# Optimization experiments

Hardware: AMD Instinct MI355X
Metric: run time of the kernel (lower is better)

Reference implementation:

```python
import jax, jax.numpy as jnp
import numpy as np

N, G, HID, LAT, E_RAND = 20000, 3000, 256, 32, 320000
EPS = 1e-8
NEG_SLOPE = 0.2  # PyG GATv2Conv default leaky_relu slope


def _segment_softmax(logits, seg, n):
    # numerically stable softmax over edges grouped by destination node
    m = jax.ops.segment_max(logits, seg, num_segments=n)
    ex = jnp.exp(logits - m[seg])
    s = jax.ops.segment_sum(ex, seg, num_segments=n)
    return ex / (s[seg] + 1e-16)


def _gatv2(x, src, dst, Wl, Wr, att, b, n):
    # GATv2 (heads=1): score = att . leaky_relu(Wl x_j + Wr x_i)
    xl = x @ Wl  # [N, C] source transform (also the message)
    xr = x @ Wr  # [N, C] destination transform
    e = jax.nn.leaky_relu(xl[src] + xr[dst], NEG_SLOPE)  # [E, C]
    logit = e @ att  # [E]
    alpha = _segment_softmax(logit, dst, n)
    out = jax.ops.segment_sum(alpha[:, None] * xl[src], dst, num_segments=n)
    return out + b


def _log_zinb(x, mu, theta, pi):
    theta = theta[None, :]
    softplus_pi = jax.nn.softplus(-pi)
    log_theta_eps = jnp.log(theta + EPS)
    log_theta_mu_eps = jnp.log(theta + mu + EPS)
    pi_theta_log = -pi + theta * (log_theta_eps - log_theta_mu_eps)
    case_zero = jax.nn.softplus(pi_theta_log) - softplus_pi
    case_nz = (-softplus_pi + pi_theta_log
               + x * (jnp.log(mu + EPS) - log_theta_mu_eps)
               + jax.lax.lgamma(x + theta) - jax.lax.lgamma(theta)
               - jax.lax.lgamma(x + 1.0))
    return jnp.where(x < EPS, case_zero, 0.0) + jnp.where(x > EPS, case_nz, 0.0)


def setup_inputs():
    key = jax.random.key(0)
    ks = jax.random.split(key, 14)
    x = jax.random.randint(ks[0], (N, G), 0, 20).astype(jnp.float32)
    er = jax.random.randint(ks[1], (2, E_RAND), 0, N, dtype=jnp.int32)
    loops = jnp.tile(jnp.arange(N, dtype=jnp.int32)[None, :], (2, 1))
    edge_index = jnp.concatenate([er, loops], axis=1)  # [2, 340000] incl self-loops
    noise = jax.random.normal(ks[2], (N, LAT), dtype=jnp.float32)

    def init(k, shape, fan_in):
        return jax.random.normal(k, shape, dtype=jnp.float32) / np.float32(np.sqrt(fan_in))

    Wl1 = init(ks[3], (G, HID), G); Wr1 = init(ks[4], (G, HID), G)
    att1 = init(ks[5], (HID,), HID); b1 = jnp.zeros((HID,), jnp.float32)
    Wl2 = init(ks[6], (HID, 2 * LAT), HID); Wr2 = init(ks[7], (HID, 2 * LAT), HID)
    att2 = init(ks[8], (2 * LAT,), 2 * LAT); b2 = jnp.zeros((2 * LAT,), jnp.float32)
    Wd1 = init(ks[9], (LAT, HID), LAT); bd1 = jnp.zeros((HID,), jnp.float32)
    Wd2 = init(ks[10], (HID, G), HID); bd2 = jnp.zeros((G,), jnp.float32)
    Wdo = init(ks[11], (HID, G), HID); bdo = jnp.zeros((G,), jnp.float32)
    theta = jax.random.uniform(ks[12], (G,), minval=0.5, maxval=2.0, dtype=jnp.float32)
    return dict(x=x, edge_index=edge_index, noise=noise,
                Wl1=Wl1, Wr1=Wr1, att1=att1, b1=b1,
                Wl2=Wl2, Wr2=Wr2, att2=att2, b2=b2,
                Wd1=Wd1, bd1=bd1, Wd2=Wd2, bd2=bd2, Wdo=Wdo, bdo=bdo,
                theta=theta)


def reference(x, edge_index, noise, Wl1, Wr1, att1, b1, Wl2, Wr2, att2, b2,
              Wd1, bd1, Wd2, bd2, Wdo, bdo, theta):
    n = x.shape[0]
    src, dst = edge_index[0], edge_index[1]
    # --- GATv2 encoder ---
    h = _gatv2(x, src, dst, Wl1, Wr1, att1, b1, n)
    h2 = _gatv2(jax.nn.relu(h), src, dst, Wl2, Wr2, att2, b2, n)  # [N, 2*LAT]
    mu_z, logvar = h2[:, :LAT], h2[:, LAT:]
    # --- reparameterize: std = sqrt(exp(logvar)) ---
    z = mu_z + noise * jnp.exp(0.5 * logvar)
    # --- ZINB decoder ---
    hd = z @ Wd1 + bd1
    mean = jax.nn.softplus(hd @ Wd2 + bd2)
    pi = hd @ Wdo + bdo
    # --- loss: -E[log ZINB] + KL(q(z|x) || N(0,I)) ---
    recon = -jnp.mean(jnp.sum(_log_zinb(x, mean, theta, pi), axis=1))
    kl = jnp.mean(0.5 * jnp.sum(mu_z ** 2 + jnp.exp(logvar) - logvar - 1.0, axis=1))
    return recon + kl
```

## Files before the change

kernel.cpp:

```cpp
#include <hip/hip_runtime.h>
#include <math.h>

#define NN   20000
#define GG   3000
#define HIDD 256
#define LATT 32
#define KP1  3008
#define FEPS 1e-8f

typedef __attribute__((ext_vector_type(8))) __bf16 bf16x8;
typedef __attribute__((ext_vector_type(4))) float f32x4;

__device__ __forceinline__ float fsp(float v) {
    float t = __expf(-fabsf(v));
    return fmaxf(v, 0.f) + __logf(1.f + t);
}
__device__ __forceinline__ float sp_approx(float t) {
    float a = fabsf(t);
    float den = fmaf(a, fmaf(a, fmaf(a, 0.8382f, -1.4958f), 1.87f), 1.f);
    return fmaxf(t, 0.f) + 0.6931472f * __builtin_amdgcn_rcpf(den);
}
__device__ __forceinline__ float lrelu(float v) {
    return v > 0.f ? v : 0.2f * v;
}
__device__ __forceinline__ ushort f2bf(float f) {
    uint b = __float_as_uint(f);
    return (ushort)((b + 0x7FFFu + ((b >> 16) & 1u)) >> 16);
}
__device__ __forceinline__ float bf2f(ushort u) {
    return __uint_as_float((uint)u << 16);
}
__device__ __forceinline__ uint pk2(float a, float b) {
    return (uint)f2bf(a) | ((uint)f2bf(b) << 16);
}
__device__ __forceinline__ void gload16(const void* g, void* l) {
    __builtin_amdgcn_global_load_lds((const __attribute__((address_space(1))) void*)g,
                                     (__attribute__((address_space(3))) void*)l, 16, 0, 0);
}

__global__ __launch_bounds__(256)
void x2bf(const float* __restrict__ x, ushort* __restrict__ xb) {
    const size_t nch = (size_t)NN * (GG / 8);
    size_t i = (size_t)blockIdx.x * 256 + threadIdx.x;
    if (i >= nch) return;
    size_t row = i / (GG / 8);
    int c8 = (int)(i % (GG / 8)) * 8;
    const float* p = x + row * GG + c8;
    float4 a = ((const float4*)p)[0];
    float4 b = ((const float4*)p)[1];
    uint4 w;
    w.x = pk2(a.x, a.y); w.y = pk2(a.z, a.w);
    w.z = pk2(b.x, b.y); w.w = pk2(b.z, b.w);
    *(uint4*)(xb + row * GG + c8) = w;
}

__global__ void zinb_table(const float* __restrict__ theta, float* __restrict__ tabL,
                           float* __restrict__ logte, int G_) {
    int idx = blockIdx.x * blockDim.x + threadIdx.x;
    if (idx >= G_ * 20) return;
    int g = idx / 20, c = idx % 20;
    float th = theta[g];
    tabL[idx] = lgammaf((float)c + th) - lgammaf(th) - lgammaf((float)c + 1.f);
    if (c == 0) logte[g] = logf(th + FEPS);
}

__global__ void edge_hist(const int* __restrict__ ei, int* __restrict__ cnt, int E) {
    int e = blockIdx.x * blockDim.x + threadIdx.x;
    if (e < E) atomicAdd(&cnt[ei[E + e]], 1);
}

__global__ __launch_bounds__(1024)
void scan_deg(int* __restrict__ cnt_cur, int* __restrict__ rowptr, int Nn) {
    __shared__ int ts[1024];
    int t = threadIdx.x;
    int chunk = (Nn + 1023) / 1024;
    int beg = t * chunk, end = min(beg + chunk, Nn);
    int s = 0;
    for (int i = beg; i < end; i++) s += cnt_cur[i];
    ts[t] = s;
    __syncthreads();
    for (int off = 1; off < 1024; off <<= 1) {
        int v = (t >= off) ? ts[t - off] : 0;
        __syncthreads();
        ts[t] += v;
        __syncthreads();
    }
    int run = (t == 0) ? 0 : ts[t - 1];
    for (int i = beg; i < end; i++) {
        int c = cnt_cur[i];
        rowptr[i] = run;
        cnt_cur[i] = run;
        run += c;
    }
    if (t == 1023) rowptr[Nn] = ts[1023];
}

__global__ void edge_scatter(const int* __restrict__ ei, int* __restrict__ cur,
                             int* __restrict__ eidx, int E) {
    int e = blockIdx.x * blockDim.x + threadIdx.x;
    if (e < E) {
        int p = atomicAdd(&cur[ei[E + e]], 1);
        eidx[p] = e;
    }
}

__global__ __launch_bounds__(256)
void transp_bf16(const float* __restrict__ in, ushort* __restrict__ out,
                 int K, int N, int Kpad) {
    __shared__ ushort t[32][33];
    int k0 = blockIdx.x * 32, n0 = blockIdx.y * 32;
    int tx = threadIdx.x & 31, ty = threadIdx.x >> 5;
    #pragma unroll
    for (int u = 0; u < 32; u += 8) {
        int k = k0 + ty + u, n = n0 + tx;
        t[ty + u][tx] = (k < K && n < N) ? f2bf(in[(size_t)k * N + n]) : (ushort)0;
    }
    __syncthreads();
    #pragma unroll
    for (int u = 0; u < 32; u += 8) {
        int n = n0 + ty + u, k = k0 + tx;
        if (n < N && k < Kpad) out[(size_t)n * Kpad + k] = t[tx][ty + u];
    }
}

__global__ __launch_bounds__(256)
void wcomb(const float* __restrict__ Wd1, const float* __restrict__ bd1,
           const float* __restrict__ Wd2, const float* __restrict__ bd2,
           const float* __restrict__ Wdo, const float* __restrict__ bdo,
           ushort* __restrict__ W2t, ushort* __restrict__ Wot,
           float* __restrict__ b2c, float* __restrict__ boc, int G_) {
    __shared__ float w1s[32 * 256];
    int tid = threadIdx.x;
    for (int i = tid; i < 32 * 256; i += 256) w1s[i] = Wd1[i];
    __syncthreads();
    int gl = tid & 63, rg = tid >> 6;
    int g = blockIdx.x * 64 + gl;
    int gc = min(g, G_ - 1);
    float a2[8], ao[8];
    #pragma unroll
    for (int i = 0; i < 8; i++) { a2[i] = 0.f; ao[i] = 0.f; }
    float ab2 = 0.f, abo = 0.f;
    for (int j = 0; j < 256; j++) {
        float w2 = Wd2[(size_t)j * G_ + gc];
        float wo = Wdo[(size_t)j * G_ + gc];
        if (rg == 0) {
            float b1 = bd1[j];
            ab2 = fmaf(b1, w2, ab2);
            abo = fmaf(b1, wo, abo);
        }
        #pragma unroll
        for (int i = 0; i < 8; i++) {
            float w1 = w1s[(rg * 8 + i) * 256 + j];
            a2[i] = fmaf(w1, w2, a2[i]);
            ao[i] = fmaf(w1, wo, ao[i]);
        }
    }
    if (g < G_) {
        #pragma unroll
        for (int i = 0; i < 8; i++) {
            W2t[(size_t)g * 32 + rg * 8 + i] = f2bf(a2[i]);
            Wot[(size_t)g * 32 + rg * 8 + i] = f2bf(ao[i]);
        }
        if (rg == 0) { b2c[g] = ab2 + bd2[g]; boc[g] = abo + bdo[g]; }
    }
}

__global__ __launch_bounds__(256, 4)
void dec_zinb(const ushort* __restrict__ zb, const ushort* __restrict__ W2t,
              const ushort* __restrict__ Wot, const ushort* __restrict__ xb,
              const float* __restrict__ tabL, const float* __restrict__ theta,
              const float* __restrict__ logte, const float* __restrict__ b2c,
              const float* __restrict__ boc, double* __restrict__ partsR,
              int M, int G_) {
    __shared__ float tabs[64 * 20];
    __shared__ float thetas[64], thltes[64], bd2s[64], bdos[64];
    __shared__ double redd[4];
    const int tid = threadIdx.x;
    const int nwg = gridDim.x * gridDim.y;
    const int orig = blockIdx.y * gridDim.x + blockIdx.x;
    const int q = nwg >> 3, r = nwg & 7, xcd = orig & 7;
    const int vv = (xcd < r ? xcd * (q + 1) : r * (q + 1) + (xcd - r) * q) + (orig >> 3);
    const int bx = vv % gridDim.x, by = vv / gridDim.x;
    const int m0 = by * 128, n0 = bx * 64;
    const int lane = tid & 63, wid = tid >> 6;
    const int wr = wid >> 1, wc = wid & 1;
    const int frow = lane & 15;
    const int ksl = (lane >> 4) << 3;

    for (int i = tid; i < 64; i += 256) {
        int g = n0 + i;
        bool ok = g < G_;
        float th = ok ? theta[g] : 1.f;
        thetas[i] = th;
        thltes[i] = ok ? th * logte[g] : 0.f;
        bd2s[i]   = ok ? b2c[g] : 0.f;
        bdos[i]   = ok ? boc[g] : 0.f;
    }
    for (int i = tid; i < 64 * 20; i += 256) {
        int g = n0 + i / 20;
        tabs[i] = (g < G_) ? tabL[(size_t)g * 20 + i % 20] : 0.f;
    }

    f32x4 acc1[4][2], acc2[4][2];
    #pragma unroll
    for (int i = 0; i < 4; i++)
        #pragma unroll
        for (int j = 0; j < 2; j++) {
            acc1[i][j] = (f32x4){0.f, 0.f, 0.f, 0.f};
            acc2[i][j] = (f32x4){0.f, 0.f, 0.f, 0.f};
        }

    bf16x8 af[4];
    #pragma unroll
    for (int mi = 0; mi < 4; mi++) {
        int gm = min(m0 + (wr << 6) + (mi << 4) + frow, M - 1);
        af[mi] = *(const bf16x8*)(zb + (size_t)gm * 32 + ksl);
    }
    #pragma unroll
    for (int ni = 0; ni < 2; ni++) {
        int gn = min(n0 + (wc << 5) + (ni << 4) + frow, G_ - 1);
        bf16x8 bf1 = *(const bf16x8*)(W2t + (size_t)gn * 32 + ksl);
        bf16x8 bf2 = *(const bf16x8*)(Wot + (size_t)gn * 32 + ksl);
        #pragma unroll
        for (int mi = 0; mi < 4; mi++) {
            acc1[mi][ni] = __builtin_amdgcn_mfma_f32_16x16x32_bf16(af[mi], bf1, acc1[mi][ni], 0, 0, 0);
            acc2[mi][ni] = __builtin_amdgcn_mfma_f32_16x16x32_bf16(af[mi], bf2, acc2[mi][ni], 0, 0, 0);
        }
    }
    __syncthreads();

    const int lr = (lane >> 4) << 2;
    float lsum = 0.f;
    #pragma unroll
    for (int mi = 0; mi < 4; mi++)
        #pragma unroll
        for (int ni = 0; ni < 2; ni++) {
            int lcol = (wc << 5) + (ni << 4) + frow;
            int gn = n0 + lcol;
            int gmb = m0 + (wr << 6) + (mi << 4) + lr;
            if (gn >= G_) continue;
            float xv4[4];
            #pragma unroll
            for (int j = 0; j < 4; j++) {
                int gm = min(gmb + j, M - 1);
                xv4[j] = bf2f(xb[(size_t)gm * G_ + gn]);
            }
            f32x4 am = acc1[mi][ni], ap = acc2[mi][ni];
            float th = thetas[lcol], thlte = thltes[lcol];
            float bm = bd2s[lcol], bp = bdos[lcol];
            #pragma unroll
            for (int j = 0; j < 4; j++) {
                if (gmb + j >= M) continue;
                float mu  = fsp(am[j] + bm);
                float pi  = ap[j] + bp;
                float spp = fsp(pi);
                float ltme = __logf(th + mu + FEPS);
                float lmu  = __logf(mu + FEPS);
                float xv = xv4[j];
                int xi = (int)(xv + 0.5f);
                float ptl = fmaf(-th, ltme, thlte) - pi;
                float corr = (xv < FEPS) ? sp_approx(-ptl) : 0.f;
                lsum += thlte + tabs[lcol * 20 + xi] - spp
                      - (th + xv) * ltme + xv * lmu + corr;
            }
        }
    #pragma unroll
    for (int off = 32; off; off >>= 1) lsum += __shfl_down(lsum, off);
    if (lane == 0) redd[wid] = (double)lsum;
    __syncthreads();
    if (tid == 0)
        partsR[by * gridDim.x + bx] = redd[0] + redd[1] + redd[2] + redd[3];
}

__global__ __launch_bounds__(512, 4)
void gemm_big(const ushort* __restrict__ At, const ushort* __restrict__ B1t,
              const ushort* __restrict__ B2t, ushort* __restrict__ C1,
              ushort* __restrict__ C2, int M, int Ka, int Kpad, int Nc) {
    __shared__ __align__(16) char lds[49152];
    char* ldsA  = lds;
    char* ldsB1 = lds + 16384;
    char* ldsB2 = lds + 32768;

    const int tid = threadIdx.x;
    const int nwg = gridDim.x * gridDim.y;
    const int orig = blockIdx.y * gridDim.x + blockIdx.x;
    const int q = nwg >> 3, r = nwg & 7, xcd = orig & 7;
    const int vv = (xcd < r ? xcd * (q + 1) : r * (q + 1) + (xcd - r) * q) + (orig >> 3);
    const int bx = vv % gridDim.x, by = vv / gridDim.x;
    const int m0 = by * 128, n0 = bx * 128;
    const int lane = tid & 63, wid = tid >> 6;
    const int wr = wid >> 2, wc = wid & 3;
    const int frow = lane & 15;
    const int fkb = (lane >> 4) << 4;

    const int row_in = lane >> 3;
    const int sch = (lane & 7) ^ (row_in & 7);
    const int ldso = (lane << 4);

    f32x4 acc1[4][2], acc2[4][2];
    #pragma unroll
    for (int i = 0; i < 4; i++)
        #pragma unroll
        for (int j = 0; j < 2; j++) {
            acc1[i][j] = (f32x4){0.f, 0.f, 0.f, 0.f};
            acc2[i][j] = (f32x4){0.f, 0.f, 0.f, 0.f};
        }

    const int nk = Kpad >> 6;
    for (int t = 0; t < nk; t++) {
        const int k0 = t << 6;
        #pragma unroll
        for (int u = 0; u < 2; u++) {
            int s = (wid << 1) + u;
            int gnb = n0 + (s << 3) + row_in;
            size_t gob = (size_t)gnb * Kpad + k0 + (sch << 3);
            gload16(B1t + gob, ldsB1 + (s << 10) + ldso);
            gload16(B2t + gob, ldsB2 + (s << 10) + ldso);
            int gma = m0 + (s << 3) + row_in;
            if (gma > M - 1) gma = M - 1;
            size_t goa = (size_t)gma * Ka + k0 + (sch << 3);
            gload16(At + goa, ldsA + (s << 10) + ldso);
        }
        __syncthreads();
        #pragma unroll
        for (int kk = 0; kk < 2; kk++) {
            int kb = (kk << 6) + fkb;
            bf16x8 af[4], b1f[2], b2f[2];
            #pragma unroll
            for (int mi = 0; mi < 4; mi++) {
                int rr = (wr << 6) + (mi << 4) + frow;
                int o = ((rr << 7) + kb) ^ ((rr & 7) << 4);
                af[mi] = *(const bf16x8*)(ldsA + o);
            }
            #pragma unroll
            for (int ni = 0; ni < 2; ni++) {
                int rr = (wc << 5) + (ni << 4) + frow;
                int o = ((rr << 7) + kb) ^ ((rr & 7) << 4);
                b1f[ni] = *(const bf16x8*)(ldsB1 + o);
                b2f[ni] = *(const bf16x8*)(ldsB2 + o);
            }
            #pragma unroll
            for (int mi = 0; mi < 4; mi++)
                #pragma unroll
                for (int ni = 0; ni < 2; ni++) {
                    acc1[mi][ni] = __builtin_amdgcn_mfma_f32_16x16x32_bf16(af[mi], b1f[ni], acc1[mi][ni], 0, 0, 0);
                    acc2[mi][ni] = __builtin_amdgcn_mfma_f32_16x16x32_bf16(af[mi], b2f[ni], acc2[mi][ni], 0, 0, 0);
                }
        }
        __syncthreads();
    }

    const int lr = (lane >> 4) << 2;
    #pragma unroll
    for (int mi = 0; mi < 4; mi++)
        #pragma unroll
        for (int ni = 0; ni < 2; ni++) {
            int gmb = m0 + (wr << 6) + (mi << 4) + lr;
            int gn  = n0 + (wc << 5) + (ni << 4) + frow;
            if (gn >= Nc) continue;
            f32x4 v1 = acc1[mi][ni], v2 = acc2[mi][ni];
            #pragma unroll
            for (int j = 0; j < 4; j++) {
                int gm = gmb + j;
                if (gm < M) {
                    C1[(size_t)gm * Nc + gn] = f2bf(v1[j]);
                    C2[(size_t)gm * Nc + gn] = f2bf(v2[j]);
                }
            }
        }
}

__global__ __launch_bounds__(256, 4)
void mfma_dual(const void* __restrict__ Ap, const ushort* __restrict__ B1t,
               const ushort* __restrict__ B2t, float* __restrict__ C1,
               float* __restrict__ C2, int M, int K, int Nc) {
    __shared__ __align__(16) char lds[24576];
    char* ldsA  = lds;
    char* ldsB1 = lds + 8192;
    char* ldsB2 = lds + 16384;

    const int tid = threadIdx.x;
    const int m0 = blockIdx.y * 64, n0 = blockIdx.x * 64;
    const int lane = tid & 63, wid = tid >> 6;
    const int wr = wid >> 1, wc = wid & 1;
    const int frow = lane & 15;
    const int fkb = (lane >> 4) << 4;

    f32x4 acc1[2][2], acc2[2][2];
    #pragma unroll
    for (int i = 0; i < 2; i++)
        #pragma unroll
        for (int j = 0; j < 2; j++) {
            acc1[i][j] = (f32x4){0.f, 0.f, 0.f, 0.f};
            acc2[i][j] = (f32x4){0.f, 0.f, 0.f, 0.f};
        }

    const int nk = (K + 63) >> 6;
    for (int t = 0; t < nk; t++) {
        const int k0 = t << 6;
        #pragma unroll
        for (int u = 0; u < 2; u++) {
            int c = tid + (u << 8);
            int row = c >> 3, col8 = (c & 7) << 3;
            int gm = m0 + row, gk = k0 + col8;
            uint4 w = make_uint4(0u, 0u, 0u, 0u);
            if (gm < M && gk < K)
                w = *(const uint4*)((const ushort*)Ap + (size_t)gm * K + gk);
            int o = ((row << 7) + (col8 << 1)) ^ ((row & 7) << 4);
            *(uint4*)(ldsA + o) = w;
        }
        #pragma unroll
        for (int u = 0; u < 2; u++) {
            int c = tid + (u << 8);
            int row = c >> 3, col8 = (c & 7) << 3;
            int gn = n0 + row, gk = k0 + col8;
            uint4 w1 = make_uint4(0u, 0u, 0u, 0u), w2 = w1;
            if (gn < Nc && gk < K) {
                size_t o = (size_t)gn * K + gk;
                w1 = *(const uint4*)(B1t + o);
                w2 = *(const uint4*)(B2t + o);
            }
            int o = ((row << 7) + (col8 << 1)) ^ ((row & 7) << 4);
            *(uint4*)(ldsB1 + o) = w1;
            *(uint4*)(ldsB2 + o) = w2;
        }
        __syncthreads();
        #pragma unroll
        for (int kk = 0; kk < 2; kk++) {
            int kb = (kk << 6) + fkb;
            bf16x8 af[2], b1f[2], b2f[2];
            #pragma unroll
            for (int mi = 0; mi < 2; mi++) {
                int rr = (wr << 5) + (mi << 4) + frow;
                int o = ((rr << 7) + kb) ^ ((rr & 7) << 4);
                af[mi] = *(const bf16x8*)(ldsA + o);
            }
            #pragma unroll
            for (int ni = 0; ni < 2; ni++) {
                int rr = (wc << 5) + (ni << 4) + frow;
                int o = ((rr << 7) + kb) ^ ((rr & 7) << 4);
                b1f[ni] = *(const bf16x8*)(ldsB1 + o);
                b2f[ni] = *(const bf16x8*)(ldsB2 + o);
            }
            #pragma unroll
            for (int mi = 0; mi < 2; mi++)
                #pragma unroll
                for (int ni = 0; ni < 2; ni++) {
                    acc1[mi][ni] = __builtin_amdgcn_mfma_f32_16x16x32_bf16(af[mi], b1f[ni], acc1[mi][ni], 0, 0, 0);
                    acc2[mi][ni] = __builtin_amdgcn_mfma_f32_16x16x32_bf16(af[mi], b2f[ni], acc2[mi][ni], 0, 0, 0);
                }
        }
        __syncthreads();
    }

    const int lr = (lane >> 4) << 2;
    #pragma unroll
    for (int mi = 0; mi < 2; mi++)
        #pragma unroll
        for (int ni = 0; ni < 2; ni++) {
            int gmb = m0 + (wr << 5) + (mi << 4) + lr;
            int gn  = n0 + (wc << 5) + (ni << 4) + frow;
            if (gn >= Nc) continue;
            f32x4 v1 = acc1[mi][ni], v2 = acc2[mi][ni];
            #pragma unroll
            for (int j = 0; j < 4; j++) {
                int gm = gmb + j;
                if (gm < M) {
                    C1[(size_t)gm * Nc + gn] = v1[j];
                    C2[(size_t)gm * Nc + gn] = v2[j];
                }
            }
        }
}

template<int DW, int OM, int IBF>
__global__ __launch_bounds__(256)
void gat_attn(const void* __restrict__ xlv, const void* __restrict__ xrv,
              const float* __restrict__ att, const int* __restrict__ ei,
              const int* __restrict__ rowptr, const int* __restrict__ eidx,
              const float* __restrict__ bias, void* __restrict__ out,
              int D, int Nn) {
    int wid = threadIdx.x >> 6, lane = threadIdx.x & 63;
    int n = blockIdx.x * 4 + wid;
    if (n >= Nn) return;
    int k = lane * DW;
    float xrr[DW], ats[DW], hacc[DW];
    if (DW == 4) {
        float4 a4 = *(const float4*)(att + k);
        ats[0] = a4.x; ats[1] = a4.y; ats[2] = a4.z; ats[3] = a4.w;
        if (IBF) {
            ushort4 u = *(const ushort4*)((const ushort*)xrv + (size_t)n * D + k);
            xrr[0] = bf2f(u.x); xrr[1] = bf2f(u.y); xrr[2] = bf2f(u.z); xrr[3] = bf2f(u.w);
        } else {
            float4 r4 = *(const float4*)((const float*)xrv + (size_t)n * D + k);
            xrr[0] = r4.x; xrr[1] = r4.y; xrr[2] = r4.z; xrr[3] = r4.w;
        }
    } else {
        ats[0] = att[k];
        xrr[0] = IBF ? bf2f(((const ushort*)xrv)[(size_t)n * D + k])
                     : ((const float*)xrv)[(size_t)n * D + k];
    }
    #pragma unroll
    for (int d = 0; d < DW; d++) hacc[d] = 0.f;
    float m = -3.0e38f, ssum = 0.f;
    int beg = rowptr[n], end = rowptr[n + 1];
    for (int j = beg; j < end; j++) {
        int e = eidx[j];
        int src = ei[e];
        float v[DW];
        float p;
        if (DW == 4) {
            if (IBF) {
                ushort4 u = *(const ushort4*)((const ushort*)xlv + (size_t)src * D + k);
                v[0] = bf2f(u.x); v[1] = bf2f(u.y); v[2] = bf2f(u.z); v[3] = bf2f(u.w);
            } else {
                float4 v4 = *(const float4*)((const float*)xlv + (size_t)src * D + k);
                v[0] = v4.x; v[1] = v4.y; v[2] = v4.z; v[3] = v4.w;
            }
            p = ats[0] * lrelu(v[0] + xrr[0]) + ats[1] * lrelu(v[1] + xrr[1])
              + ats[2] * lrelu(v[2] + xrr[2]) + ats[3] * lrelu(v[3] + xrr[3]);
        } else {
            v[0] = IBF ? bf2f(((const ushort*)xlv)[(size_t)src * D + k])
                       : ((const float*)xlv)[(size_t)src * D + k];
            p = ats[0] * lrelu(v[0] + xrr[0]);
        }
        #pragma unroll
        for (int o2 = 32; o2; o2 >>= 1) p += __shfl_xor(p, o2);
        float mnew = fmaxf(m, p);
        float sc = __expf(m - mnew);
        float w  = __expf(p - mnew);
        ssum = fmaf(ssum, sc, w);
        #pragma unroll
        for (int d = 0; d < DW; d++) hacc[d] = fmaf(hacc[d], sc, w * v[d]);
        m = mnew;
    }
    float inv = 1.f / (ssum + 1e-16f);
    if (DW == 4) {
        float4 b = *(const float4*)(bias + k);
        float r0 = fmaf(hacc[0], inv, b.x), r1 = fmaf(hacc[1], inv, b.y);
        float r2 = fmaf(hacc[2], inv, b.z), r3 = fmaf(hacc[3], inv, b.w);
        if (OM == 0) {
            *(float4*)((float*)out + (size_t)n * D + k) = make_float4(r0, r1, r2, r3);
        } else {
            ushort4 o;
            o.x = f2bf(fmaxf(r0, 0.f)); o.y = f2bf(fmaxf(r1, 0.f));
            o.z = f2bf(fmaxf(r2, 0.f)); o.w = f2bf(fmaxf(r3, 0.f));
            *(ushort4*)((ushort*)out + (size_t)n * D + k) = o;
        }
    } else {
        float r0 = fmaf(hacc[0], inv, bias[k]);
        if (OM == 0) ((float*)out)[(size_t)n * D + k] = r0;
        else         ((ushort*)out)[(size_t)n * D + k] = f2bf(fmaxf(r0, 0.f));
    }
}

__global__ __launch_bounds__(256)
void z_kl(const float* __restrict__ h2, const float* __restrict__ noise,
          ushort* __restrict__ z, double* __restrict__ partsK, int Nn) {
    __shared__ double rd[4];
    int gid = blockIdx.x * blockDim.x + threadIdx.x;
    int n = gid >> 5, k = gid & 31;
    float kt = 0.f;
    if (n < Nn) {
        float mu = h2[(size_t)n * 64 + k];
        float lv = h2[(size_t)n * 64 + 32 + k];
        float ev = expf(lv);
        z[(size_t)n * 32 + k] = f2bf(mu + noise[(size_t)n * 32 + k] * expf(0.5f * lv));
        kt = 0.5f * (mu * mu + ev - lv - 1.f);
    }
    #pragma unroll
    for (int off = 32; off; off >>= 1) kt += __shfl_down(kt, off);
    int wid = threadIdx.x >> 6, lane = threadIdx.x & 63;
    if (lane == 0) rd[wid] = (double)kt;
    __syncthreads();
    if (threadIdx.x == 0) partsK[blockIdx.x] = rd[0] + rd[1] + rd[2] + rd[3];
}

__global__ __launch_bounds__(256)
void final_reduce(const double* __restrict__ pR, int nR,
                  const double* __restrict__ pK, int nK,
                  float* __restrict__ out, int Nn) {
    __shared__ double sd[256];
    double s = 0.0;
    for (int i = threadIdx.x; i < nR; i += 256) s -= pR[i];
    for (int i = threadIdx.x; i < nK; i += 256) s += pK[i];
    sd[threadIdx.x] = s;
    __syncthreads();
    for (int o = 128; o; o >>= 1) {
        if (threadIdx.x < o) sd[threadIdx.x] += sd[threadIdx.x + o];
        __syncthreads();
    }
    if (threadIdx.x == 0) out[0] = (float)(sd[0] / (double)Nn);
}

extern "C" void kernel_launch(void* const* d_in, const int* in_sizes, int n_in,
                              void* d_out, int out_size, void* d_ws, size_t ws_size,
                              hipStream_t stream) {
    const int N_ = NN, G_ = GG, HID_ = HIDD;
    const float* x     = (const float*)d_in[0];
    const int*   ei    = (const int*)d_in[1];
    const float* noise = (const float*)d_in[2];
    const float* Wl1   = (const float*)d_in[3];
    const float* Wr1   = (const float*)d_in[4];
    const float* att1  = (const float*)d_in[5];
    const float* b1    = (const float*)d_in[6];
    const float* Wl2   = (const float*)d_in[7];
    const float* Wr2   = (const float*)d_in[8];
    const float* att2  = (const float*)d_in[9];
    const float* b2    = (const float*)d_in[10];
    const float* Wd1   = (const float*)d_in[11];
    const float* bd1   = (const float*)d_in[12];
    const float* Wd2   = (const float*)d_in[13];
    const float* bd2   = (const float*)d_in[14];
    const float* Wdo   = (const float*)d_in[15];
    const float* bdo   = (const float*)d_in[16];
    const float* theta = (const float*)d_in[17];
    const int E = in_sizes[1] / 2;

    const int MB128 = (N_ + 127) / 128;
    const int DGX   = (G_ + 63) / 64;
    const int nR    = DGX * MB128;
    const int nKb   = (N_ * 32) / 256;

    char* base = (char*)d_ws;
    size_t off = 0;
    auto alloc = [&](size_t bytes) -> char* {
        char* p = base + off;
        off = (off + bytes + 255) & ~(size_t)255;
        return p;
    };
    double* partsR = (double*)alloc((size_t)nR * 8);
    double* partsK = (double*)alloc((size_t)nKb * 8);
    float*  tabL  = (float*)alloc((size_t)G_ * 20 * 4);
    float*  logte = (float*)alloc((size_t)G_ * 4);
    int*    rowptr= (int*)alloc((size_t)(N_ + 1) * 4);
    int*    cur   = (int*)alloc((size_t)N_ * 4);
    int*    eidx  = (int*)alloc((size_t)E * 4);
    ushort* Wl1t  = (ushort*)alloc((size_t)HID_ * KP1 * 2);
    ushort* Wr1t  = (ushort*)alloc((size_t)HID_ * KP1 * 2);
    ushort* Wl2t  = (ushort*)alloc((size_t)64 * HID_ * 2);
    ushort* Wr2t  = (ushort*)alloc((size_t)64 * HID_ * 2);
    ushort* W2t   = (ushort*)alloc((size_t)G_ * 32 * 2);
    ushort* Wot   = (ushort*)alloc((size_t)G_ * 32 * 2);
    float*  b2c   = (float*)alloc((size_t)G_ * 4);
    float*  boc   = (float*)alloc((size_t)G_ * 4);
    ushort* xb    = (ushort*)alloc((size_t)N_ * G_ * 2);
    ushort* xl1b  = (ushort*)alloc((size_t)N_ * HID_ * 2);
    ushort* xr1b  = (ushort*)alloc((size_t)N_ * HID_ * 2);
    ushort* h_bf  = (ushort*)alloc((size_t)N_ * HID_ * 2);
    float*  xl2 = (float*)xl1b;
    float*  xr2 = xl2 + (size_t)N_ * 64;
    float*  h2  = xr2 + (size_t)N_ * 64;
    ushort* zb  = (ushort*)(h2 + (size_t)N_ * 64);

    float*  outf = (float*)d_out;

    hipMemsetAsync(cur, 0, N_ * sizeof(int), stream);

    x2bf<<<(int)(((size_t)N_ * (G_ / 8) + 255) / 256), 256, 0, stream>>>(x, xb);
    zinb_table<<<(G_ * 20 + 255) / 256, 256, 0, stream>>>(theta, tabL, logte, G_);
    edge_hist<<<(E + 255) / 256, 256, 0, stream>>>(ei, cur, E);
    scan_deg<<<1, 1024, 0, stream>>>(cur, rowptr, N_);
    edge_scatter<<<(E + 255) / 256, 256, 0, stream>>>(ei, cur, eidx, E);

    transp_bf16<<<dim3(KP1 / 32, (HID_ + 31) / 32), 256, 0, stream>>>(Wl1, Wl1t, G_, HID_, KP1);
    transp_bf16<<<dim3(KP1 / 32, (HID_ + 31) / 32), 256, 0, stream>>>(Wr1, Wr1t, G_, HID_, KP1);
    transp_bf16<<<dim3(HID_ / 32, 2), 256, 0, stream>>>(Wl2, Wl2t, HID_, 64, HID_);
    transp_bf16<<<dim3(HID_ / 32, 2), 256, 0, stream>>>(Wr2, Wr2t, HID_, 64, HID_);

    wcomb<<<(G_ + 63) / 64, 256, 0, stream>>>(
        Wd1, bd1, Wd2, bd2, Wdo, bdo, W2t, Wot, b2c, boc, G_);

    gemm_big<<<dim3(HID_ / 128, MB128), 512, 0, stream>>>(
        xb, Wl1t, Wr1t, xl1b, xr1b, N_, G_, KP1, HID_);
    gat_attn<4, 1, 1><<<(N_ + 3) / 4, 256, 0, stream>>>(
        xl1b, xr1b, att1, ei, rowptr, eidx, b1, h_bf, HID_, N_);

    mfma_dual<<<dim3(1, (N_ + 63) / 64), 256, 0, stream>>>(
        h_bf, Wl2t, Wr2t, xl2, xr2, N_, HID_, 64);
    gat_attn<1, 0, 0><<<(N_ + 3) / 4, 256, 0, stream>>>(
        xl2, xr2, att2, ei, rowptr, eidx, b2, h2, 64, N_);

    z_kl<<<nKb, 256, 0, stream>>>(h2, noise, zb, partsK, N_);

    dec_zinb<<<dim3(DGX, MB128), 256, 0, stream>>>(
        zb, W2t, Wot, xb, tabL, theta, logte, b2c, boc, partsR, N_, G_);

    final_reduce<<<1, 256, 0, stream>>>(partsR, nR, partsK, nKb, outf, N_);
}
```

Before: 630.9 us.

## Pad bf16 x to KP1 columns and stage decoder x tile via async LDS loads

```diff
diff --git a/kernel.cpp b/kernel.cpp
--- a/kernel.cpp
+++ b/kernel.cpp
@@ -40,18 +40,20 @@
 
 __global__ __launch_bounds__(256)
 void x2bf(const float* __restrict__ x, ushort* __restrict__ xb) {
-    const size_t nch = (size_t)NN * (GG / 8);
+    const int CH = KP1 / 8;
     size_t i = (size_t)blockIdx.x * 256 + threadIdx.x;
-    if (i >= nch) return;
-    size_t row = i / (GG / 8);
-    int c8 = (int)(i % (GG / 8)) * 8;
-    const float* p = x + row * GG + c8;
-    float4 a = ((const float4*)p)[0];
-    float4 b = ((const float4*)p)[1];
-    uint4 w;
-    w.x = pk2(a.x, a.y); w.y = pk2(a.z, a.w);
-    w.z = pk2(b.x, b.y); w.w = pk2(b.z, b.w);
-    *(uint4*)(xb + row * GG + c8) = w;
+    if (i >= (size_t)NN * CH) return;
+    size_t row = i / CH;
+    int c8 = (int)(i % CH) * 8;
+    uint4 w = make_uint4(0u, 0u, 0u, 0u);
+    if (c8 < GG) {
+        const float* p = x + row * GG + c8;
+        float4 a = ((const float4*)p)[0];
+        float4 b = ((const float4*)p)[1];
+        w.x = pk2(a.x, a.y); w.y = pk2(a.z, a.w);
+        w.z = pk2(b.x, b.y); w.w = pk2(b.z, b.w);
+    }
+    *(uint4*)(xb + row * KP1 + c8) = w;
 }
 
 __global__ void zinb_table(const float* __restrict__ theta, float* __restrict__ tabL,
@@ -165,13 +167,14 @@
     }
 }
 
-__global__ __launch_bounds__(256, 4)
+__global__ __launch_bounds__(256, 8)
 void dec_zinb(const ushort* __restrict__ zb, const ushort* __restrict__ W2t,
               const ushort* __restrict__ Wot, const ushort* __restrict__ xb,
               const float* __restrict__ tabL, const float* __restrict__ theta,
               const float* __restrict__ logte, const float* __restrict__ b2c,
               const float* __restrict__ boc, double* __restrict__ partsR,
               int M, int G_) {
+    __shared__ __align__(16) char xs[16384];
     __shared__ float tabs[64 * 20];
     __shared__ float thetas[64], thltes[64], bd2s[64], bdos[64];
     __shared__ double redd[4];
@@ -187,6 +190,20 @@
     const int frow = lane & 15;
     const int ksl = (lane >> 4) << 3;
 
+    {
+        const int row_in8 = lane >> 3;
+        const int ch = lane & 7;
+        #pragma unroll
+        for (int u = 0; u < 4; u++) {
+            int s = (wid << 2) + u;
+            int rr = (s << 3) + row_in8;
+            int gm = m0 + rr; if (gm > M - 1) gm = M - 1;
+            int csw = ch ^ (rr & 7);
+            size_t go = (size_t)gm * KP1 + n0 + (csw << 3);
+            gload16(xb + go, xs + (s << 10) + (lane << 4));
+        }
+    }
+
     for (int i = tid; i < 64; i += 256) {
         int g = n0 + i;
         bool ok = g < G_;
@@ -237,26 +254,22 @@
         for (int ni = 0; ni < 2; ni++) {
             int lcol = (wc << 5) + (ni << 4) + frow;
             int gn = n0 + lcol;
-            int gmb = m0 + (wr << 6) + (mi << 4) + lr;
+            int lrow0 = (wr << 6) + (mi << 4) + lr;
             if (gn >= G_) continue;
-            float xv4[4];
-            #pragma unroll
-            for (int j = 0; j < 4; j++) {
-                int gm = min(gmb + j, M - 1);
-                xv4[j] = bf2f(xb[(size_t)gm * G_ + gn]);
-            }
             f32x4 am = acc1[mi][ni], ap = acc2[mi][ni];
             float th = thetas[lcol], thlte = thltes[lcol];
             float bm = bd2s[lcol], bp = bdos[lcol];
             #pragma unroll
             for (int j = 0; j < 4; j++) {
-                if (gmb + j >= M) continue;
+                int lrow = lrow0 + j;
+                if (m0 + lrow >= M) continue;
+                int o = (lrow << 7) + ((((lcol >> 3) ^ (lrow & 7)) << 4)) + ((lcol & 7) << 1);
+                float xv = bf2f(*(const ushort*)(xs + o));
                 float mu  = fsp(am[j] + bm);
                 float pi  = ap[j] + bp;
                 float spp = fsp(pi);
                 float ltme = __logf(th + mu + FEPS);
                 float lmu  = __logf(mu + FEPS);
-                float xv = xv4[j];
                 int xi = (int)(xv + 0.5f);
                 float ptl = fmaf(-th, ltme, thlte) - pi;
                 float corr = (xv < FEPS) ? sp_approx(-ptl) : 0.f;
@@ -275,7 +288,7 @@
 __global__ __launch_bounds__(512, 4)
 void gemm_big(const ushort* __restrict__ At, const ushort* __restrict__ B1t,
               const ushort* __restrict__ B2t, ushort* __restrict__ C1,
-              ushort* __restrict__ C2, int M, int Ka, int Kpad, int Nc) {
+              ushort* __restrict__ C2, int M, int Kpad, int Nc) {
     __shared__ __align__(16) char lds[49152];
     char* ldsA  = lds;
     char* ldsB1 = lds + 16384;
@@ -318,7 +331,7 @@
             gload16(B2t + gob, ldsB2 + (s << 10) + ldso);
             int gma = m0 + (s << 3) + row_in;
             if (gma > M - 1) gma = M - 1;
-            size_t goa = (size_t)gma * Ka + k0 + (sch << 3);
+            size_t goa = (size_t)gma * Kpad + k0 + (sch << 3);
             gload16(At + goa, ldsA + (s << 10) + ldso);
         }
         __syncthreads();
@@ -644,7 +657,7 @@
     ushort* Wot   = (ushort*)alloc((size_t)G_ * 32 * 2);
     float*  b2c   = (float*)alloc((size_t)G_ * 4);
     float*  boc   = (float*)alloc((size_t)G_ * 4);
-    ushort* xb    = (ushort*)alloc((size_t)N_ * G_ * 2);
+    ushort* xb    = (ushort*)alloc((size_t)N_ * KP1 * 2);
     ushort* xl1b  = (ushort*)alloc((size_t)N_ * HID_ * 2);
     ushort* xr1b  = (ushort*)alloc((size_t)N_ * HID_ * 2);
     ushort* h_bf  = (ushort*)alloc((size_t)N_ * HID_ * 2);
@@ -657,7 +670,7 @@
 
     hipMemsetAsync(cur, 0, N_ * sizeof(int), stream);
 
-    x2bf<<<(int)(((size_t)N_ * (G_ / 8) + 255) / 256), 256, 0, stream>>>(x, xb);
+    x2bf<<<(int)(((size_t)N_ * (KP1 / 8) + 255) / 256), 256, 0, stream>>>(x, xb);
     zinb_table<<<(G_ * 20 + 255) / 256, 256, 0, stream>>>(theta, tabL, logte, G_);
     edge_hist<<<(E + 255) / 256, 256, 0, stream>>>(ei, cur, E);
     scan_deg<<<1, 1024, 0, stream>>>(cur, rowptr, N_);
@@ -672,7 +685,7 @@
         Wd1, bd1, Wd2, bd2, Wdo, bdo, W2t, Wot, b2c, boc, G_);
 
     gemm_big<<<dim3(HID_ / 128, MB128), 512, 0, stream>>>(
-        xb, Wl1t, Wr1t, xl1b, xr1b, N_, G_, KP1, HID_);
+        xb, Wl1t, Wr1t, xl1b, xr1b, N_, KP1, HID_);
     gat_attn<4, 1, 1><<<(N_ + 3) / 4, 256, 0, stream>>>(
         xl1b, xr1b, att1, ei, rowptr, eidx, b1, h_bf, HID_, N_);
 
```

Result: slower. 644.3 us (+2.1%).
